# Kernel tuning notes

Hardware: AMD Instinct MI355X
Metric: run time of the kernel (lower is better)

The kernel has to match this reference:

```python
import jax, jax.numpy as jnp
import numpy as np

M = 30000          # number of internal octree nodes
N = 2              # branching factor per axis (N3Tree)
S = N ** 3         # children per node
D = 32             # data_dim
DEPTH_LIMIT = 10
MLP_RATIO = 2
L = 7 * M + 1      # number of leaf cells: 8*M - (M-1)


def _build_tree(seed=0):
    """Random recursive octree: parent_pack[i] = packed (parent_node,x,y,z) of node i."""
    rng = np.random.default_rng(seed)
    parent_pack = np.zeros(M, np.int32)
    node_depth = np.zeros(M, np.int32)
    occupied = np.zeros((M, S), bool)
    free = [(0, c) for c in range(S)]  # refinable cells (keeps child depth <= DEPTH_LIMIT-1)
    for i in range(1, M):
        j = int(rng.integers(len(free)))
        p, c = free[j]
        free[j] = free[-1]
        free.pop()
        occupied[p, c] = True
        parent_pack[i] = p * S + c
        node_depth[i] = node_depth[p] + 1
        if node_depth[i] <= DEPTH_LIMIT - 2:
            free.extend((i, c2) for c2 in range(S))
    leaf_idx = np.flatnonzero(~occupied.reshape(-1)).astype(np.int32)
    assert leaf_idx.shape[0] == L
    return parent_pack, node_depth, leaf_idx


def setup_inputs() -> dict:
    parent_pack, node_depth, leaf_idx = _build_tree()
    # torch.sort(parent_depth, dim=0, descending=True) sorts each column independently
    idx_sorted = np.sort(parent_pack)[::-1].copy()
    depth_sorted = np.sort(node_depth)[::-1].copy()
    key = jax.random.key(0)
    ks = jax.random.split(key, 8)
    H = D * MLP_RATIO
    return {
        "data": jax.random.normal(ks[0], (M, N, N, N, D), jnp.float32),
        "conv_w": jax.random.normal(ks[1], (DEPTH_LIMIT, D, D, S), jnp.float32) * 0.05,
        "conv_b": jnp.zeros((DEPTH_LIMIT, D), jnp.float32),
        "depth_weight": jnp.arange(1, DEPTH_LIMIT + 1, dtype=jnp.float32) / (DEPTH_LIMIT + 1),
        "hf_w1": jax.random.normal(ks[2], (D, H), jnp.float32) * 0.02,
        "hf_b1": jnp.zeros((H,), jnp.float32),
        "hf_w2": jax.random.normal(ks[3], (H, 3), jnp.float32) * 0.02,
        "hf_b2": jnp.zeros((3,), jnp.float32),
        "hs_w1": jax.random.normal(ks[4], (D, H), jnp.float32) * 0.02,
        "hs_b1": jnp.zeros((H,), jnp.float32),
        "hs_w2": jax.random.normal(ks[5], (H, 1), jnp.float32) * 0.02,
        "hs_b2": jnp.zeros((1,), jnp.float32),
        "idx_sorted": jnp.asarray(idx_sorted),
        "depth_sorted": jnp.asarray(depth_sorted),
        "node_depth": jnp.asarray(node_depth),
        "leaf_idx": jnp.asarray(leaf_idx),
    }


def _mlp(x, w1, b1, w2, b2):
    # timm Mlp (Linear-GELU-Drop-Linear-Drop), dropout is identity in eval
    return jax.nn.gelu(x @ w1 + b1, approximate=False) @ w2 + b2


def reference(data, conv_w, conv_b, depth_weight,
              hf_w1, hf_b1, hf_w2, hf_b2,
              hs_w1, hs_b1, hs_w2, hs_b2,
              idx_sorted, depth_sorted, node_depth, leaf_idx):
    Dd = data.shape[-1]

    def step(carry, inp):
        dat, feats = carry
        idx, dsort = inp
        p = idx // S
        cell = idx % S
        x, y, z = cell // (N * N), (cell // N) % N, cell % N
        blk = dat[p].reshape(S, Dd)            # [(N1 N2 N3), D]
        cd = node_depth[p]                     # conv chosen by node's own depth entry
        # TreeConv over the 8-cell block: y[o] = sum_{i,k} W[o,i,k] * x[i,k] + b[o]
        feat = jnp.einsum('oik,ki->o', conv_w[cd], blk) + conv_b[cd]
        dat = dat.at[p, x, y, z].set(feat)     # recursive scatter write into tree.data
        feats = feats + depth_weight[dsort] * feat
        return (dat, feats), None

    (data, feats), _ = jax.lax.scan(
        step, (data, jnp.zeros((Dd,), data.dtype)), (idx_sorted, depth_sorted))

    leaves = data.reshape(-1, Dd)[leaf_idx] + feats   # tree[:] + features, [L, D]
    f = _mlp(leaves, hf_w1, hf_b1, hf_w2, hf_b2)      # [L, 3]
    sigma = _mlp(leaves, hs_w1, hs_b1, hs_w2, hs_b2)  # [L, 1]
    return jnp.concatenate([f, sigma], axis=1)        # [L, 4]
```

## Files before the change

kernel.cpp:

```cpp
#include <hip/hip_runtime.h>
#include <hip/hip_bf16.h>
#include <math.h>


typedef __attribute__((ext_vector_type(8))) short short8;
typedef __attribute__((ext_vector_type(4))) float f32x4;

#define WT_N 81920
#define RCAP 30720
#define RSTRIDE 32

__device__ __forceinline__ unsigned short f2bf(float x) {
    __hip_bfloat16 h = __float2bfloat16(x);
    return *reinterpret_cast<unsigned short*>(&h);
}
__device__ __forceinline__ float bf2f(unsigned short h) {
    union { float f; unsigned u; } v; v.u = ((unsigned)h) << 16;
    return v.f;
}

__device__ __forceinline__ float4 shfl4(float4 v, int src) {
    float4 r;
    r.x = __shfl(v.x, src, 64);
    r.y = __shfl(v.y, src, 64);
    r.z = __shfl(v.z, src, 64);
    r.w = __shfl(v.w, src, 64);
    return r;
}

__device__ __forceinline__ void red_ig(float4& T) {
    #pragma unroll
    for (int m = 8; m <= 32; m <<= 1) {
        T.x += __shfl_xor(T.x, m, 64);
        T.y += __shfl_xor(T.y, m, 64);
        T.z += __shfl_xor(T.z, m, 64);
        T.w += __shfl_xor(T.w, m, 64);
    }
}

__device__ __forceinline__ float gelu_fast(float x)
{
    float e = __expf(-1.702f * x);
    return x * __builtin_amdgcn_rcpf(1.0f + e);
}

__global__ __launch_bounds__(256) void prep_kernel(
    const float* __restrict__ conv_w, float* __restrict__ Wt,
    const float* __restrict__ hf_w1, const float* __restrict__ hs_w1,
    short* __restrict__ bph, short* __restrict__ bpl,
    const int* __restrict__ idx_sorted, const int* __restrict__ node_depth,
    int* __restrict__ gcnt, int2* __restrict__ runlist, int M)
{
    __shared__ float tl[32 * 257];
    __shared__ int hcnt[16], hbase[16];

    if (blockIdx.x < 10) {
        int d = blockIdx.x;
        int base = d * 8192;
        for (int t = threadIdx.x; t < 8192; t += 256)
            tl[(t >> 8) * 257 + (t & 255)] = conv_w[base + t];
        __syncthreads();
        for (int t = threadIdx.x; t < 8192; t += 256) {
            int o = t & 31, i = (t >> 5) & 31, k = t >> 10;
            Wt[base + t] = tl[o * 257 + i * 8 + k];
        }
        return;
    }

    if (threadIdx.x < 16) hcnt[threadIdx.x] = 0;
    __syncthreads();

    int j = (blockIdx.x - 10) * 256 + threadIdx.x;
    bool start = false;
    int d = 0, myp = 0, mypos = 0;

    if (j < M) {
        int p = idx_sorted[j] >> 3;
        start = (j == 0) || ((idx_sorted[j - 1] >> 3) != p);
        if (start) {
            d = node_depth[p];
            myp = p;
            mypos = atomicAdd(&hcnt[d], 1);
        }
    } else if (j < M + 512) {
        int jj = j - M;
        int lane = jj & 63;
        int q = jj >> 6;
        int m = q >> 2, tq = q & 3;
        int kg = lane >> 4, n0 = lane & 15, k0 = kg * 8;
        const float* __restrict__ w1 = m ? hs_w1 : hf_w1;
        #pragma unroll
        for (int i = 0; i < 8; ++i) {
            float w = w1[(k0 + i) * 64 + tq * 16 + n0];
            unsigned short hh = f2bf(w);
            bph[(q * 64 + lane) * 8 + i] = (short)hh;
            bpl[(q * 64 + lane) * 8 + i] = (short)f2bf(w - bf2f(hh));
        }
    }

    __syncthreads();
    if (threadIdx.x < 16) {
        int c = hcnt[threadIdx.x];
        if (c > 0) hbase[threadIdx.x] = atomicAdd(&gcnt[threadIdx.x * RSTRIDE], c);
    }
    __syncthreads();
    if (start) runlist[d * RCAP + hbase[d] + mypos] = make_int2(j, myp);
}

__device__ __forceinline__ void run_steps(
    float4& T, float4& blk, float4& pfs, int ec, float edw, int base16,
    int n, int p, bool valid, const float* __restrict__ W, float4 bias,
    int og, int og8, int ig, float* __restrict__ patch)
{
    if (!valid) return;
    int c = __shfl(ec, base16, 64);
    float4 wc0 = *(const float4*)(W + (c * 32 + ig * 4 + 0) * 32 + og);
    float4 wc1 = *(const float4*)(W + (c * 32 + ig * 4 + 1) * 32 + og);
    float4 wc2 = *(const float4*)(W + (c * 32 + ig * 4 + 2) * 32 + og);
    float4 wc3 = *(const float4*)(W + (c * 32 + ig * 4 + 3) * 32 + og);

    for (int s = 0;; ++s) {
        float dw = __shfl(edw, base16 + s, 64);
        float4 feat = {T.x + bias.x, T.y + bias.y, T.z + bias.z, T.w + bias.w};
        pfs.x = fmaf(dw, feat.x, pfs.x); pfs.y = fmaf(dw, feat.y, pfs.y);
        pfs.z = fmaf(dw, feat.z, pfs.z); pfs.w = fmaf(dw, feat.w, pfs.w);

        if (s + 1 == n) {
            if (p == 0 && c == 0 && ig == 0)
                *(float4*)(patch + og) = feat;
            return;
        }

        int cn = __shfl(ec, base16 + s + 1, 64);
        float4 nw0 = *(const float4*)(W + (cn * 32 + ig * 4 + 0) * 32 + og);
        float4 nw1 = *(const float4*)(W + (cn * 32 + ig * 4 + 1) * 32 + og);
        float4 nw2 = *(const float4*)(W + (cn * 32 + ig * 4 + 2) * 32 + og);
        float4 nw3 = *(const float4*)(W + (cn * 32 + ig * 4 + 3) * 32 + og);

        float4 ov = shfl4(blk, c * 8 + og8);
        float4 du = {feat.x - ov.x, feat.y - ov.y, feat.z - ov.z, feat.w - ov.w};
        if (ig == c) blk = feat;
        float4 u = shfl4(du, og8 * 8 + ig);

        float4 a4;
        a4.x = u.x * wc0.x; a4.y = u.x * wc0.y;
        a4.z = u.x * wc0.z; a4.w = u.x * wc0.w;
        a4.x = fmaf(u.y, wc1.x, a4.x); a4.y = fmaf(u.y, wc1.y, a4.y);
        a4.z = fmaf(u.y, wc1.z, a4.z); a4.w = fmaf(u.y, wc1.w, a4.w);
        a4.x = fmaf(u.z, wc2.x, a4.x); a4.y = fmaf(u.z, wc2.y, a4.y);
        a4.z = fmaf(u.z, wc2.z, a4.z); a4.w = fmaf(u.z, wc2.w, a4.w);
        a4.x = fmaf(u.w, wc3.x, a4.x); a4.y = fmaf(u.w, wc3.y, a4.y);
        a4.z = fmaf(u.w, wc3.z, a4.z); a4.w = fmaf(u.w, wc3.w, a4.w);
        red_ig(a4);
        T.x += a4.x; T.y += a4.y; T.z += a4.z; T.w += a4.w;

        c = cn;
        wc0 = nw0; wc1 = nw1; wc2 = nw2; wc3 = nw3;
    }
}

#define FMA16(T, X) \
    T.x = fmaf(X.x, w0.x, T.x); T.y = fmaf(X.x, w0.y, T.y); \
    T.z = fmaf(X.x, w0.z, T.z); T.w = fmaf(X.x, w0.w, T.w); \
    T.x = fmaf(X.y, w1.x, T.x); T.y = fmaf(X.y, w1.y, T.y); \
    T.z = fmaf(X.y, w1.z, T.z); T.w = fmaf(X.y, w1.w, T.w); \
    T.x = fmaf(X.z, w2.x, T.x); T.y = fmaf(X.z, w2.y, T.y); \
    T.z = fmaf(X.z, w2.z, T.z); T.w = fmaf(X.z, w2.w, T.w); \
    T.x = fmaf(X.w, w3.x, T.x); T.y = fmaf(X.w, w3.y, T.y); \
    T.z = fmaf(X.w, w3.z, T.z); T.w = fmaf(X.w, w3.w, T.w);

__global__ __launch_bounds__(256, 4) void conv_scan(
    const float* __restrict__ data, const float* __restrict__ Wt,
    const float* __restrict__ conv_b, const float* __restrict__ depth_weight,
    const int* __restrict__ idx_sorted, const int* __restrict__ depth_sorted,
    const int* __restrict__ gcnt, const int2* __restrict__ runlist,
    float* __restrict__ feats_part, float* __restrict__ patch, int M)
{
    int w = (blockIdx.x * 256 + threadIdx.x) >> 6;
    int l = threadIdx.x & 63;
    int og8 = l & 7, og = og8 * 4, ig = l >> 3;
    int q = l >> 4;

    int acc = 0, d = -1, chunk = 0, cnt = 0;
    #pragma unroll
    for (int dd = 0; dd < 10; ++dd) {
        int c = gcnt[dd * RSTRIDE];
        int nw = (c + 3) >> 2;
        if (d < 0 && w < acc + nw) { d = dd; chunk = w - acc; cnt = c; }
        acc += nw;
    }
    if (d < 0) return;

    int r0 = chunk * 4;
    int rq = r0 + q; if (rq >= cnt) rq = cnt - 1;
    int2 e = runlist[d * RCAP + rq];
    int t0l = e.x, pl = e.y;

    int wl = l & 15;
    int tw = t0l + wl;
    int twc = tw < M ? tw : M - 1;
    int iw  = idx_sorted[twc];
    int dsw = depth_sorted[twc];
    unsigned long long mask = __ballot((tw < M) && ((iw >> 3) == pl));
    int   ec  = iw & 7;
    float edw = depth_weight[dsw & 15];

    const float* __restrict__ W = Wt + d * 8192;
    const float4 bias = *(const float4*)(conv_b + d * 32 + og);

    int p0 = __shfl(pl, 0, 64),  p1 = __shfl(pl, 16, 64),
        p2 = __shfl(pl, 32, 64), p3 = __shfl(pl, 48, 64);
    int n0 = __builtin_ctz(~(unsigned)( mask        & 0xFFFFull));
    int n1 = __builtin_ctz(~(unsigned)((mask >> 16) & 0xFFFFull));
    int n2 = __builtin_ctz(~(unsigned)((mask >> 32) & 0xFFFFull));
    int n3 = __builtin_ctz(~(unsigned)((mask >> 48) & 0xFFFFull));
    bool v0 = (r0 + 0 < cnt), v1 = (r0 + 1 < cnt),
         v2 = (r0 + 2 < cnt), v3 = (r0 + 3 < cnt);

    float4 B0 = *(const float4*)(data + (size_t)p0 * 256 + ig * 32 + og);
    float4 B1 = *(const float4*)(data + (size_t)p1 * 256 + ig * 32 + og);
    float4 B2 = *(const float4*)(data + (size_t)p2 * 256 + ig * 32 + og);
    float4 B3 = *(const float4*)(data + (size_t)p3 * 256 + ig * 32 + og);

    float4 T0 = {0,0,0,0}, T1 = {0,0,0,0}, T2 = {0,0,0,0}, T3 = {0,0,0,0};
    #pragma unroll
    for (int k = 0; k < 8; ++k) {
        const float4 w0 = *(const float4*)(W + (k * 32 + ig * 4 + 0) * 32 + og);
        const float4 w1 = *(const float4*)(W + (k * 32 + ig * 4 + 1) * 32 + og);
        const float4 w2 = *(const float4*)(W + (k * 32 + ig * 4 + 2) * 32 + og);
        const float4 w3 = *(const float4*)(W + (k * 32 + ig * 4 + 3) * 32 + og);
        int src = k * 8 + ig;
        float4 x0 = shfl4(B0, src), x1 = shfl4(B1, src),
               x2 = shfl4(B2, src), x3 = shfl4(B3, src);
        FMA16(T0, x0); FMA16(T1, x1); FMA16(T2, x2); FMA16(T3, x3);
    }
    red_ig(T0); red_ig(T1); red_ig(T2); red_ig(T3);

    float4 pfs = {0,0,0,0};
    run_steps(T0, B0, pfs, ec, edw,  0, n0, p0, v0, W, bias, og, og8, ig, patch);
    run_steps(T1, B1, pfs, ec, edw, 16, n1, p1, v1, W, bias, og, og8, ig, patch);
    run_steps(T2, B2, pfs, ec, edw, 32, n2, p2, v2, W, bias, og, og8, ig, patch);
    run_steps(T3, B3, pfs, ec, edw, 48, n3, p3, v3, W, bias, og, og8, ig, patch);

    if (ig == 0) {
        float* fp = feats_part + ((w & 63) * 32) + og;
        atomicAdd(fp + 0, pfs.x);
        atomicAdd(fp + 1, pfs.y);
        atomicAdd(fp + 2, pfs.z);
        atomicAdd(fp + 3, pfs.w);
    }
}

__global__ __launch_bounds__(256, 4) void mlp_kernel(
    const float* __restrict__ data, const float* __restrict__ feats_part,
    const float* __restrict__ patch, const int* __restrict__ leaf_idx,
    const short* __restrict__ bph, const short* __restrict__ bpl,
    const float* __restrict__ hf_b1, const float* __restrict__ hf_w2,
    const float* __restrict__ hf_b2, const float* __restrict__ hs_b1,
    const float* __restrict__ hs_w2, const float* __restrict__ hs_b2,
    float* __restrict__ out, int L)
{
    __shared__ float red[256];
    __shared__ float sh_fts[32];
    {
        int ch = threadIdx.x & 31, g = threadIdx.x >> 5;
        float s = 0.f;
        #pragma unroll
        for (int j = 0; j < 8; ++j) s += feats_part[(g + j * 8) * 32 + ch];
        red[threadIdx.x] = s;
        __syncthreads();
        if (threadIdx.x < 128) red[threadIdx.x] += red[threadIdx.x + 128];
        __syncthreads();
        if (threadIdx.x < 64) red[threadIdx.x] += red[threadIdx.x + 64];
        __syncthreads();
        if (threadIdx.x < 32)
            sh_fts[threadIdx.x] = red[threadIdx.x] + red[threadIdx.x + 32];
        __syncthreads();
    }

    int l = threadIdx.x & 63;
    int ck = blockIdx.x * 4 + (threadIdx.x >> 6);
    int nchunks = (L + 63) >> 6;
    if (ck >= nchunks) return;
    int base = ck * 64;
    int n0 = l & 15, kg = l >> 4, k0 = kg * 8;

    float fts[8];
    #pragma unroll
    for (int i = 0; i < 8; ++i) fts[i] = sh_fts[k0 + i];

    float w2r[16], b1r[8];
    #pragma unroll
    for (int t = 0; t < 4; ++t) {
        int h = t * 16 + n0;
        w2r[t * 4 + 0] = hf_w2[h * 3 + 0];
        w2r[t * 4 + 1] = hf_w2[h * 3 + 1];
        w2r[t * 4 + 2] = hf_w2[h * 3 + 2];
        w2r[t * 4 + 3] = hs_w2[h];
        b1r[t]     = hf_b1[h];
        b1r[4 + t] = hs_b1[h];
    }
    float b20 = hf_b2[0], b21 = hf_b2[1], b22 = hf_b2[2], b23 = hs_b2[0];

    #pragma unroll
    for (int tm = 0; tm < 4; ++tm) {
        int r  = base + tm * 16 + n0;
        int rc = r < L ? r : L - 1;
        int row = leaf_idx[rc];
        const float* __restrict__ src = (row == 0) ? patch : (data + (size_t)row * 32);
        float4 vA = *(const float4*)(src + k0);
        float4 vB = *(const float4*)(src + k0 + 4);
        float xv[8] = {vA.x, vA.y, vA.z, vA.w, vB.x, vB.y, vB.z, vB.w};
        short8 ahi, alo;
        #pragma unroll
        for (int i = 0; i < 8; ++i) {
            float x = xv[i] + fts[i];
            unsigned short hh = f2bf(x);
            ahi[i] = (short)hh;
            alo[i] = (short)f2bf(x - bf2f(hh));
        }

        f32x4 acc[8];
        #pragma unroll
        for (int qq = 0; qq < 8; ++qq) {
            short8 bh = *(const short8*)(bph + (qq * 64 + l) * 8);
            short8 bl = *(const short8*)(bpl + (qq * 64 + l) * 8);
            float bv = b1r[qq >= 4 ? 4 + (qq - 4) : qq];
            f32x4 a = (f32x4){bv, bv, bv, bv};
            a = __builtin_amdgcn_mfma_f32_16x16x32_bf16(ahi, bh, a, 0, 0, 0);
            a = __builtin_amdgcn_mfma_f32_16x16x32_bf16(alo, bh, a, 0, 0, 0);
            a = __builtin_amdgcn_mfma_f32_16x16x32_bf16(ahi, bl, a, 0, 0, 0);
            acc[qq] = a;
        }

        float o[4][4];
        #pragma unroll
        for (int g2 = 0; g2 < 4; ++g2) {
            #pragma unroll
            for (int c = 0; c < 4; ++c) o[g2][c] = 0.f;
        }
        #pragma unroll
        for (int t = 0; t < 4; ++t) {
            #pragma unroll
            for (int reg = 0; reg < 4; ++reg) {
                float gf = gelu_fast(acc[t][reg]);
                float gs = gelu_fast(acc[4 + t][reg]);
                o[reg][0] = fmaf(gf, w2r[t * 4 + 0], o[reg][0]);
                o[reg][1] = fmaf(gf, w2r[t * 4 + 1], o[reg][1]);
                o[reg][2] = fmaf(gf, w2r[t * 4 + 2], o[reg][2]);
                o[reg][3] = fmaf(gs, w2r[t * 4 + 3], o[reg][3]);
            }
        }
        #pragma unroll
        for (int mk = 1; mk < 16; mk <<= 1) {
            #pragma unroll
            for (int reg = 0; reg < 4; ++reg) {
                #pragma unroll
                for (int c = 0; c < 4; ++c)
                    o[reg][c] += __shfl_xor(o[reg][c], mk, 64);
            }
        }
        if (n0 < 4) {
            int rL = base + tm * 16 + kg * 4 + n0;
            if (rL < L) {
                float s0 = n0 == 0 ? o[0][0] : n0 == 1 ? o[1][0] : n0 == 2 ? o[2][0] : o[3][0];
                float s1 = n0 == 0 ? o[0][1] : n0 == 1 ? o[1][1] : n0 == 2 ? o[2][1] : o[3][1];
                float s2 = n0 == 0 ? o[0][2] : n0 == 1 ? o[1][2] : n0 == 2 ? o[2][2] : o[3][2];
                float s3 = n0 == 0 ? o[0][3] : n0 == 1 ? o[1][3] : n0 == 2 ? o[2][3] : o[3][3];
                float4 res = {s0 + b20, s1 + b21, s2 + b22, s3 + b23};
                *(float4*)(out + (size_t)rL * 4) = res;
            }
        }
    }
}

extern "C" void kernel_launch(void* const* d_in, const int* in_sizes, int n_in,
                              void* d_out, int out_size, void* d_ws, size_t ws_size,
                              hipStream_t stream)
{
    const float* data         = (const float*)d_in[0];
    const float* conv_w       = (const float*)d_in[1];
    const float* conv_b       = (const float*)d_in[2];
    const float* depth_weight = (const float*)d_in[3];
    const float* hf_w1        = (const float*)d_in[4];
    const float* hf_b1        = (const float*)d_in[5];
    const float* hf_w2        = (const float*)d_in[6];
    const float* hf_b2        = (const float*)d_in[7];
    const float* hs_w1        = (const float*)d_in[8];
    const float* hs_b1        = (const float*)d_in[9];
    const float* hs_w2        = (const float*)d_in[10];
    const float* hs_b2        = (const float*)d_in[11];
    const int*   idx_sorted   = (const int*)d_in[12];
    const int*   depth_sorted = (const int*)d_in[13];
    const int*   node_depth   = (const int*)d_in[14];
    const int*   leaf_idx     = (const int*)d_in[15];

    int M = in_sizes[12];
    int L = in_sizes[15];
    float* out = (float*)d_out;

    float* Wt         = (float*)d_ws;
    float* patch      = Wt + WT_N;
    short* bph        = (short*)(patch + 32);
    short* bpl        = bph + 4096;
    int*   gcnt       = (int*)(bpl + 4096);
    float* feats_part = (float*)(gcnt + 10 * RSTRIDE);
    int2*  runlist    = (int2*)(feats_part + 64 * 32);

    hipMemsetAsync(gcnt, 0, 10 * RSTRIDE * sizeof(int) + 64 * 32 * sizeof(float),
                   stream);

    int nb_prep = 10 + (M + 512 + 255) / 256;
    prep_kernel<<<nb_prep, 256, 0, stream>>>(
        conv_w, Wt, hf_w1, hs_w1, bph, bpl,
        idx_sorted, node_depth, gcnt, runlist, M);

    int max_waves = (M + 3) / 4 + 10;
    conv_scan<<<(max_waves + 3) / 4, 256, 0, stream>>>(
        data, Wt, conv_b, depth_weight, idx_sorted, depth_sorted,
        gcnt, runlist, feats_part, patch, M);

    int nchunks = (L + 63) / 64;
    mlp_kernel<<<(nchunks + 3) / 4, 256, 0, stream>>>(
        data, feats_part, patch, leaf_idx, bph, bpl,
        hf_b1, hf_w2, hf_b2, hs_b1, hs_w2, hs_b2, out, L);
}
```

Before: 64.97 us.

## Fold feats into first-layer bias and drop split-bf16 MFMAs for non-patch rows

The global feature vector is now multiplied by W1 once per block and added to the first-layer bias, instead of being added to every leaf input before the matmul. Waves whose rows contain no patched row then use a single bf16 MFMA per tile instead of the three-MFMA hi/lo split. The high-precision weights are also staged in shared memory. This cuts MFMA work and global weight loads in the MLP kernel, at the cost of lower precision (bf16 inputs and weights only) for most rows, plus extra per-block setup and shared-memory use.

```diff
diff --git a/kernel.cpp b/kernel.cpp
--- a/kernel.cpp
+++ b/kernel.cpp
@@ -255,6 +255,7 @@
     const float* __restrict__ data, const float* __restrict__ feats_part,
     const float* __restrict__ patch, const int* __restrict__ leaf_idx,
     const short* __restrict__ bph, const short* __restrict__ bpl,
+    const float* __restrict__ hf_w1, const float* __restrict__ hs_w1,
     const float* __restrict__ hf_b1, const float* __restrict__ hf_w2,
     const float* __restrict__ hf_b2, const float* __restrict__ hs_b1,
     const float* __restrict__ hs_w2, const float* __restrict__ hs_b2,
@@ -262,6 +263,9 @@
 {
     __shared__ float red[256];
     __shared__ float sh_fts[32];
+    __shared__ float sh_fvec[128];
+    __shared__ __align__(16) short sh_b[4096];
+
     {
         int ch = threadIdx.x & 31, g = threadIdx.x >> 5;
         float s = 0.f;
@@ -275,6 +279,22 @@
         __syncthreads();
         if (threadIdx.x < 32)
             sh_fts[threadIdx.x] = red[threadIdx.x] + red[threadIdx.x + 32];
+        __syncthreads();
+    }
+
+    {
+        const int4* src = (const int4*)bph;
+        int4* dst = (int4*)sh_b;
+        for (int t = threadIdx.x; t < 512; t += 256) dst[t] = src[t];
+
+        if (threadIdx.x < 128) {
+            int m = threadIdx.x >> 6, h = threadIdx.x & 63;
+            const float* __restrict__ w1 = m ? hs_w1 : hf_w1;
+            float s = 0.f;
+            #pragma unroll
+            for (int k = 0; k < 32; ++k) s = fmaf(sh_fts[k], w1[k * 64 + h], s);
+            sh_fvec[threadIdx.x] = s;
+        }
         __syncthreads();
     }
 
@@ -284,10 +304,6 @@
     if (ck >= nchunks) return;
     int base = ck * 64;
     int n0 = l & 15, kg = l >> 4, k0 = kg * 8;
-
-    float fts[8];
-    #pragma unroll
-    for (int i = 0; i < 8; ++i) fts[i] = sh_fts[k0 + i];
 
     float w2r[16], b1r[8];
     #pragma unroll
@@ -297,8 +313,8 @@
         w2r[t * 4 + 1] = hf_w2[h * 3 + 1];
         w2r[t * 4 + 2] = hf_w2[h * 3 + 2];
         w2r[t * 4 + 3] = hs_w2[h];
-        b1r[t]     = hf_b1[h];
-        b1r[4 + t] = hs_b1[h];
+        b1r[t]     = hf_b1[h] + sh_fvec[h];
+        b1r[4 + t] = hs_b1[h] + sh_fvec[64 + h];
     }
     float b20 = hf_b2[0], b21 = hf_b2[1], b22 = hf_b2[2], b23 = hs_b2[0];
 
@@ -311,26 +327,38 @@
         float4 vA = *(const float4*)(src + k0);
         float4 vB = *(const float4*)(src + k0 + 4);
         float xv[8] = {vA.x, vA.y, vA.z, vA.w, vB.x, vB.y, vB.z, vB.w};
-        short8 ahi, alo;
-        #pragma unroll
-        for (int i = 0; i < 8; ++i) {
-            float x = xv[i] + fts[i];
-            unsigned short hh = f2bf(x);
-            ahi[i] = (short)hh;
-            alo[i] = (short)f2bf(x - bf2f(hh));
-        }
+        short8 ahi;
+        #pragma unroll
+        for (int i = 0; i < 8; ++i) ahi[i] = (short)f2bf(xv[i]);
 
         f32x4 acc[8];
-        #pragma unroll
-        for (int qq = 0; qq < 8; ++qq) {
-            short8 bh = *(const short8*)(bph + (qq * 64 + l) * 8);
-            short8 bl = *(const short8*)(bpl + (qq * 64 + l) * 8);
-            float bv = b1r[qq >= 4 ? 4 + (qq - 4) : qq];
-            f32x4 a = (f32x4){bv, bv, bv, bv};
-            a = __builtin_amdgcn_mfma_f32_16x16x32_bf16(ahi, bh, a, 0, 0, 0);
-            a = __builtin_amdgcn_mfma_f32_16x16x32_bf16(alo, bh, a, 0, 0, 0);
-            a = __builtin_amdgcn_mfma_f32_16x16x32_bf16(ahi, bl, a, 0, 0, 0);
-            acc[qq] = a;
+        bool anyPatch = __any(row == 0);
+        if (!anyPatch) {
+            #pragma unroll
+            for (int qq = 0; qq < 8; ++qq) {
+                short8 bh = *(const short8*)(sh_b + (qq * 64 + l) * 8);
+                float bv = b1r[qq];
+                f32x4 a = (f32x4){bv, bv, bv, bv};
+                acc[qq] = __builtin_amdgcn_mfma_f32_16x16x32_bf16(ahi, bh, a, 0, 0, 0);
+            }
+        } else {
+            short8 alo;
+            #pragma unroll
+            for (int i = 0; i < 8; ++i) {
+                unsigned short hh = (unsigned short)ahi[i];
+                alo[i] = (short)f2bf(xv[i] - bf2f(hh));
+            }
+            #pragma unroll
+            for (int qq = 0; qq < 8; ++qq) {
+                short8 bh = *(const short8*)(sh_b + (qq * 64 + l) * 8);
+                short8 bl = *(const short8*)(bpl + (qq * 64 + l) * 8);
+                float bv = b1r[qq];
+                f32x4 a = (f32x4){bv, bv, bv, bv};
+                a = __builtin_amdgcn_mfma_f32_16x16x32_bf16(ahi, bh, a, 0, 0, 0);
+                a = __builtin_amdgcn_mfma_f32_16x16x32_bf16(alo, bh, a, 0, 0, 0);
+                a = __builtin_amdgcn_mfma_f32_16x16x32_bf16(ahi, bl, a, 0, 0, 0);
+                acc[qq] = a;
+            }
         }
 
         float o[4][4];
@@ -423,5 +451,6 @@
     int nchunks = (L + 63) / 64;
     mlp_kernel<<<(nchunks + 3) / 4, 256, 0, stream>>>(
         data, feats_part, patch, leaf_idx, bph, bpl,
+        hf_w1, hs_w1,
         hf_b1, hf_w2, hf_b2, hs_b1, hs_w2, hs_b2, out, L);
 }
```

New measurement: 58.36 us. 10.2% less time.
